# Optimization experiments

Measured on AMD Instinct MI355X. Metric: run time of the kernel, lower is better.

## Reference

```python
import jax, jax.numpy as jnp
import numpy as np

B, T, D, H = 512, 128, 128, 2048  # batch, seq_len, input/output dim, hidden dim
W_SCALE = 0.02


def setup_inputs() -> dict:
    key = jax.random.key(0)
    ks = jax.random.split(key, 4)
    return {
        "tgt": jax.random.normal(ks[0], (B, T, D), jnp.float32),
        "W_ih": jax.random.normal(ks[1], (4 * H, D), jnp.float32) * W_SCALE,
        "W_hh": jax.random.normal(ks[2], (4 * H, H), jnp.float32) * W_SCALE,
        "b_ih": jnp.zeros((4 * H,), jnp.float32),
        "b_hh": jnp.zeros((4 * H,), jnp.float32),
        "W_out": jax.random.normal(ks[3], (D, H), jnp.float32) * W_SCALE,
        "b_out": jnp.zeros((D,), jnp.float32),
    }


def reference(tgt, W_ih, W_hh, b_ih, b_hh, W_out, b_out):
    # LSTMDecoder.forward with teacher_forcing_ratio=0.0 (deterministic,
    # tgt: [B, T, D]; first frame tgt[:, 0] seeds the decoder.
    batch, max_len, _ = tgt.shape
    hidden = W_hh.shape[1]
    b = b_ih + b_hh  # fuse the two LSTM biases

    def step(carry, _):
        x, h, c = carry
        # torch nn.LSTM gate order: i, f, g, o
        gates = x @ W_ih.T + h @ W_hh.T + b  # [B, 4H]
        i, f, g, o = jnp.split(gates, 4, axis=-1)
        c = jax.nn.sigmoid(f) * c + jax.nn.sigmoid(i) * jnp.tanh(g)
        h = jax.nn.sigmoid(o) * jnp.tanh(c)
        out = h @ W_out.T + b_out  # [B, D]
        return (out, h, c), out

    h0 = jnp.zeros((batch, hidden), tgt.dtype)
    c0 = jnp.zeros((batch, hidden), tgt.dtype)
    _, outs = jax.lax.scan(step, (tgt[:, 0, :], h0, c0), None, length=max_len)
    return outs.transpose(1, 0, 2)  # [B, T, D]
```

## Files before the change

kernel.cpp:

```cpp
#include <hip/hip_runtime.h>
#include <hip/hip_fp16.h>

typedef _Float16 f16;
typedef __attribute__((ext_vector_type(8))) _Float16 f16x8;
typedef __attribute__((ext_vector_type(16))) float f32x16;

#define GLL(src, dst) __builtin_amdgcn_global_load_lds( \
    (const __attribute__((address_space(1))) void*)(src), \
    (__attribute__((address_space(3))) void*)(dst), 16, 0, 0)

__device__ __forceinline__ size_t foff(int r, int k, int nkb) {
    return ((size_t)((r >> 5) * nkb + (k >> 4)) << 9)
         + (size_t)(((((k >> 3) & 1)) << 8) + ((r & 31) << 3) + (k & 7));
}

__device__ __forceinline__ void rgemm(
    const f16* __restrict__ pA,
    const f16* __restrict__ pB0, const f16* __restrict__ pB1,
    f16* sB, int wv, int lane, int n, f32x16 acc[2])
{
    #pragma unroll
    for (int nt = 0; nt < 2; ++nt)
      #pragma unroll
      for (int e = 0; e < 16; ++e)
        acc[nt][e] = 0.f;

    const f16* pBs = (wv >> 1) ? pB1 : pB0;
    const int jb = (wv & 1) * 2;
    f16* dst0 = sB + (wv >> 1) * 2048 + jb * 512;

    f16x8 X[4], Y[4];
    auto LA = [&](f16x8 (&R)[4], int t) {
        size_t o = (size_t)t * 2048;
        R[0] = *(const f16x8*)(pA + o);
        R[1] = *(const f16x8*)(pA + o + 512);
        R[2] = *(const f16x8*)(pA + o + 1024);
        R[3] = *(const f16x8*)(pA + o + 1536);
    };
    auto BG = [&](int buf, int t) {
        size_t o = (size_t)t * 2048 + (size_t)jb * 512;
        GLL(pBs + o,       dst0 + buf * 4096);
        GLL(pBs + o + 512, dst0 + buf * 4096 + 512);
    };
    auto STEP = [&](f16x8 (&R)[4], int buf, int t, bool last) {
        if (last) asm volatile("s_waitcnt vmcnt(0)" ::: "memory");
        else      asm volatile("s_waitcnt vmcnt(6)" ::: "memory");
        __builtin_amdgcn_sched_barrier(0);
        __builtin_amdgcn_s_barrier();
        __builtin_amdgcn_sched_barrier(0);
        f16x8 bf[2][4];
        const f16* bb = sB + buf * 4096 + lane * 8;
        #pragma unroll
        for (int nt = 0; nt < 2; ++nt)
          #pragma unroll
          for (int kk = 0; kk < 4; ++kk)
            bf[nt][kk] = *(const f16x8*)(bb + nt * 2048 + kk * 512);
        asm volatile("s_waitcnt lgkmcnt(0)" ::: "memory");
        __builtin_amdgcn_sched_barrier(0);
        __builtin_amdgcn_s_barrier();
        __builtin_amdgcn_sched_barrier(0);
        if (t + 2 < n) BG(buf, t + 2);
        __builtin_amdgcn_s_setprio(1);
        #pragma unroll
        for (int kk = 0; kk < 4; ++kk)
          #pragma unroll
          for (int nt = 0; nt < 2; ++nt)
            acc[nt] = __builtin_amdgcn_mfma_f32_32x32x16_f16(
                R[kk], bf[nt][kk], acc[nt], 0, 0, 0);
        __builtin_amdgcn_s_setprio(0);
        if (t + 2 < n) LA(R, t + 2);
    };

    __builtin_amdgcn_sched_barrier(0);
    BG(0, 0); LA(X, 0);
    __builtin_amdgcn_sched_barrier(0);
    BG(1, 1); LA(Y, 1);
    __builtin_amdgcn_sched_barrier(0);
    for (int t = 0; t < n; t += 2) {
        STEP(X, 0, t, false);
        STEP(Y, 1, t + 1, t + 2 >= n);
    }
}

#define PICKV(ii) ((ii) == 0 ? w0[e] : (ii) == 1 ? w1[e] : (ii) == 2 ? w2[e] : w3[e])

__global__ __launch_bounds__(256, 2) void k_step(
    const f16* __restrict__ Af, int nkb,
    const f16* __restrict__ Bf,
    const float* __restrict__ bias,
    float* __restrict__ Cst,
    f16* __restrict__ Hout)
{
    __shared__ alignas(16) f16 sB[8192];
    const int P = blockIdx.x;
    const int L = (P & 7) * ((int)gridDim.x >> 3) + (P >> 3);
    const int cg = L >> 2, rg = L & 3;
    const int tid = threadIdx.x;
    const int wv = tid >> 6, lane = tid & 63;
    const int l31 = lane & 31, hi = lane >> 5;
    const int mb = rg * 4 + wv;
    const f16* pA  = Af + ((size_t)mb * nkb) * 512 + lane * 8;
    const f16* pB0 = Bf + ((size_t)(cg * 2) * nkb) * 512 + lane * 8;
    const f16* pB1 = pB0 + (size_t)nkb * 512;
    f32x16 acc[2];
    rgemm(pA, pB0, pB1, sB, wv, lane, nkb >> 2, acc);

    const int g = l31 & 3;
    #pragma unroll
    for (int nt = 0; nt < 2; ++nt) {
        const int hid = cg * 16 + nt * 8 + (l31 >> 2);
        const float bown = bias[(g << 11) + hid];
        float w0[16], w1[16], w2[16], w3[16];
        #pragma unroll
        for (int e = 0; e < 16; ++e) {
            float x = acc[nt][e] + bown;
            float xx = (g == 2) ? 2.f * x : x;
            float s = 1.f / (1.f + __expf(-xx));
            w0[e] = (g == 2) ? 2.f * s - 1.f : s;
        }
        #pragma unroll
        for (int e = 0; e < 16; ++e) {
            w1[e] = __shfl_xor(w0[e], 1);
            w2[e] = __shfl_xor(w0[e], 2);
            w3[e] = __shfl_xor(w0[e], 3);
        }
        const int rowb = rg * 128 + wv * 32 + 4 * hi;
        #pragma unroll
        for (int eg = 0; eg < 4; ++eg) {
            if (g == eg) {
                #pragma unroll
                for (int q = 0; q < 4; ++q) {
                    const int e = eg * 4 + q;
                    const float iv = PICKV(eg ^ 0);
                    const float fv = PICKV(eg ^ 1);
                    const float gv = PICKV(eg ^ 2);
                    const float ov = PICKV(eg ^ 3);
                    const int row = rowb + q + 8 * eg;
                    const size_t cidx = (size_t)row * 2048 + hid;
                    const float c = fv * Cst[cidx] + iv * gv;
                    Cst[cidx] = c;
                    Hout[foff(row, hid, 128)] = (f16)(ov * tanhf(c));
                }
            }
        }
    }
}

__global__ __launch_bounds__(256, 2) void k_out(
    const f16* __restrict__ Hbase, const f16* __restrict__ Bf,
    const float* __restrict__ bout, float* __restrict__ out,
    int t0, int rgshift)
{
    __shared__ alignas(16) f16 sB[8192];
    const int P = blockIdx.x;
    const int L = (P & 7) * ((int)gridDim.x >> 3) + (P >> 3);
    const int cg = L >> rgshift;
    const int rg = L & ((1 << rgshift) - 1);
    const int tid = threadIdx.x;
    const int wv = tid >> 6, lane = tid & 63;
    const int l31 = lane & 31, hi = lane >> 5;
    const int m0 = rg * 128 + wv * 32;
    const int slot = m0 >> 9, mloc32 = (m0 & 511) >> 5;
    const f16* pA  = Hbase + (size_t)slot * 1048576
                   + ((size_t)mloc32 * 128) * 512 + lane * 8;
    const f16* pB0 = Bf + ((size_t)(cg * 2) * 128) * 512 + lane * 8;
    const f16* pB1 = pB0 + (size_t)128 * 512;
    f32x16 acc[2];
    rgemm(pA, pB0, pB1, sB, wv, lane, 32, acc);

    #pragma unroll
    for (int nt = 0; nt < 2; ++nt) {
        const int d = cg * 64 + nt * 32 + l31;
        const float bo = bout[d];
        #pragma unroll
        for (int e = 0; e < 16; ++e) {
            const int m = m0 + (e & 3) + 8 * (e >> 2) + 4 * hi;
            out[(size_t)(m & 511) * 16384 + (size_t)(t0 + (m >> 9)) * 128 + d]
                = acc[nt][e] + bo;
        }
    }
}

__global__ __launch_bounds__(256, 2) void k_wcomb(
    const f16* __restrict__ Af,
    const f16* __restrict__ Bf,
    const float* __restrict__ Whh, f16* __restrict__ Wf)
{
    __shared__ alignas(16) f16 sB[8192];
    const int P = blockIdx.x;
    const int L = (P & 7) * ((int)gridDim.x >> 3) + (P >> 3);
    const int cg = L >> 6, rg = L & 63;
    const int tid = threadIdx.x;
    const int wv = tid >> 6, lane = tid & 63;
    const int l31 = lane & 31, hi = lane >> 5;
    const int mb = rg * 4 + wv;
    const f16* pA  = Af + ((size_t)mb * 8) * 512 + lane * 8;
    const f16* pB0 = Bf + ((size_t)(cg * 2) * 8) * 512 + lane * 8;
    const f16* pB1 = pB0 + (size_t)8 * 512;
    f32x16 acc[2];
    rgemm(pA, pB0, pB1, sB, wv, lane, 2, acc);

    #pragma unroll
    for (int nt = 0; nt < 2; ++nt) {
        const int kc = cg * 64 + nt * 32 + l31;
        #pragma unroll
        for (int e = 0; e < 16; ++e) {
            const int r = rg * 128 + wv * 32 + (e & 3) + 8 * (e >> 2) + 4 * hi;
            const float v = acc[nt][e] + Whh[(size_t)r * 2048 + kc];
            const int rho = ((r & 2047) << 2) | (r >> 11);
            Wf[foff(rho, kc, 128)] = (f16)v;
        }
    }
}


__global__ void k_x0f(const float* __restrict__ tgt, f16* __restrict__ x0f)
{
    int i = blockIdx.x * 256 + threadIdx.x;
    int b = i >> 7, k = i & 127;
    x0f[foff(b, k, 8)] = (f16)tgt[(size_t)b * 16384 + k];
}

__global__ void k_wihf(const float* __restrict__ Wih, f16* __restrict__ Wihf)
{
    int i = blockIdx.x * 256 + threadIdx.x;
    int rho = i >> 7, k = i & 127;
    int gate = rho & 3, hid = rho >> 2;
    Wihf[foff(rho, k, 8)] = (f16)Wih[((size_t)gate * 2048 + hid) * 128 + k];
}

__global__ void k_wihaf(const float* __restrict__ Wih, f16* __restrict__ Wihaf)
{
    int i = blockIdx.x * 256 + threadIdx.x;
    int r = i >> 7, k = i & 127;
    Wihaf[foff(r, k, 8)] = (f16)Wih[(size_t)r * 128 + k];
}

__global__ void k_woutTf(const float* __restrict__ Wout, f16* __restrict__ WoutTf)
{
    int i = blockIdx.x * 256 + threadIdx.x;
    int d = i >> 11, n = i & 2047;
    WoutTf[foff(n, d, 8)] = (f16)Wout[(size_t)d * 2048 + n];
}

__global__ void k_woutf(const float* __restrict__ Wout, f16* __restrict__ Woutf)
{
    int i = blockIdx.x * 256 + threadIdx.x;
    int d = i >> 11, k = i & 2047;
    Woutf[foff(d, k, 128)] = (f16)Wout[(size_t)d * 2048 + k];
}

__global__ void k_bias(const float* __restrict__ bih, const float* __restrict__ bhh,
                       const float* __restrict__ Wih, const float* __restrict__ bout,
                       float* __restrict__ b0, float* __restrict__ bp)
{
    int r = blockIdx.x * 256 + threadIdx.x;
    if (r >= 8192) return;
    float s = bih[r] + bhh[r];
    float a = 0.f;
    for (int d = 0; d < 128; ++d) a += Wih[(size_t)r * 128 + d] * bout[d];
    b0[r] = s;
    bp[r] = s + a;
}


extern "C" void kernel_launch(void* const* d_in, const int* in_sizes, int n_in,
                              void* d_out, int out_size, void* d_ws, size_t ws_size,
                              hipStream_t stream)
{
    const float* tgt  = (const float*)d_in[0];
    const float* Wih  = (const float*)d_in[1];
    const float* Whh  = (const float*)d_in[2];
    const float* bih  = (const float*)d_in[3];
    const float* bhh  = (const float*)d_in[4];
    const float* Wout = (const float*)d_in[5];
    const float* bout = (const float*)d_in[6];
    float* out = (float*)d_out;

    char* ws = (char*)d_ws;
    size_t off = 0;
    auto alloc = [&](size_t bytes) -> void* {
        void* p = ws + off;
        off += (bytes + 255) & ~(size_t)255;
        return p;
    };
    f16*   Wf     = (f16*)alloc((size_t)8192 * 2048 * 2);
    f16*   Wihf   = (f16*)alloc((size_t)8192 * 128 * 2);
    f16*   Wihaf  = (f16*)alloc((size_t)8192 * 128 * 2);
    f16*   WoutTf = (f16*)alloc((size_t)2048 * 128 * 2);
    f16*   Woutf  = (f16*)alloc((size_t)128 * 2048 * 2);
    f16*   x0f    = (f16*)alloc((size_t)512 * 128 * 2);
    float* b0     = (float*)alloc(8192 * 4);
    float* bp     = (float*)alloc(8192 * 4);
    float* Cst    = (float*)alloc((size_t)512 * 2048 * 4);

    const size_t slotsz = (size_t)512 * 2048;
    int depth = 0;
    const int cands[7] = {128, 64, 32, 16, 8, 4, 2};
    for (int i = 0; i < 7; ++i)
        if (off + (size_t)cands[i] * slotsz * 2 <= ws_size) { depth = cands[i]; break; }
    if (depth == 0) return;
    f16* Hbuf = (f16*)alloc((size_t)depth * slotsz * 2);
    const int rgshift = __builtin_ctz((unsigned)(depth * 4));

    hipMemsetAsync(Cst, 0, (size_t)512 * 2048 * 4, stream);
    k_x0f   <<<dim3(256),  dim3(256), 0, stream>>>(tgt, x0f);
    k_wihf  <<<dim3(4096), dim3(256), 0, stream>>>(Wih, Wihf);
    k_wihaf <<<dim3(4096), dim3(256), 0, stream>>>(Wih, Wihaf);
    k_woutTf<<<dim3(1024), dim3(256), 0, stream>>>(Wout, WoutTf);
    k_woutf <<<dim3(1024), dim3(256), 0, stream>>>(Wout, Woutf);
    k_bias  <<<dim3(32),   dim3(256), 0, stream>>>(bih, bhh, Wih, bout, b0, bp);
    k_wcomb <<<dim3(2048), dim3(256), 0, stream>>>(Wihaf, WoutTf, Whh, Wf);

    k_step<<<dim3(512), dim3(256), 0, stream>>>(x0f, 8, Wihf, b0, Cst, Hbuf);
    for (int s = 1; s < 128; ++s) {
        if ((s % depth) == 0)
            k_out<<<dim3(8 * depth), dim3(256), 0, stream>>>(
                Hbuf, Woutf, bout, out, s - depth, rgshift);
        k_step<<<dim3(512), dim3(256), 0, stream>>>(
            Hbuf + (size_t)((s - 1) % depth) * slotsz, 128, Wf, bp,
            Cst, Hbuf + (size_t)(s % depth) * slotsz);
    }
    k_out<<<dim3(8 * depth), dim3(256), 0, stream>>>(
        Hbuf, Woutf, bout, out, 128 - depth, rgshift);
}
```

Baseline: 4.538 ms.

## Deepen GEMM software pipeline to four LDS buffers with a single barrier

The inner recurrent GEMM moves from a 2-stage to a 4-stage pipeline. It uses four register sets for A fragments and four LDS buffers for B tiles, prefetching 3–4 k-steps ahead. The second workgroup barrier per step is removed, since the buffer being refilled is no longer the one being read. LDS per block doubles to 32 KB and register pressure rises, which could lower occupancy or cause spills. Any benefit depends on how much latency was still exposed in the memory-bound recurrent step.

Result: faster. 4.408 ms (-2.9%).

```diff
diff --git a/kernel.cpp b/kernel.cpp
--- a/kernel.cpp
+++ b/kernel.cpp
@@ -8,6 +8,7 @@
 #define GLL(src, dst) __builtin_amdgcn_global_load_lds( \
     (const __attribute__((address_space(1))) void*)(src), \
     (__attribute__((address_space(3))) void*)(dst), 16, 0, 0)
+#define SB0() __builtin_amdgcn_sched_barrier(0)
 
 __device__ __forceinline__ size_t foff(int r, int k, int nkb) {
     return ((size_t)((r >> 5) * nkb + (k >> 4)) << 9)
@@ -29,7 +30,7 @@
     const int jb = (wv & 1) * 2;
     f16* dst0 = sB + (wv >> 1) * 2048 + jb * 512;
 
-    f16x8 X[4], Y[4];
+    f16x8 R0[4], R1[4], R2[4], R3[4];
     auto LA = [&](f16x8 (&R)[4], int t) {
         size_t o = (size_t)t * 2048;
         R[0] = *(const f16x8*)(pA + o);
@@ -42,12 +43,17 @@
         GLL(pBs + o,       dst0 + buf * 4096);
         GLL(pBs + o + 512, dst0 + buf * 4096 + 512);
     };
-    auto STEP = [&](f16x8 (&R)[4], int buf, int t, bool last) {
-        if (last) asm volatile("s_waitcnt vmcnt(0)" ::: "memory");
-        else      asm volatile("s_waitcnt vmcnt(6)" ::: "memory");
-        __builtin_amdgcn_sched_barrier(0);
+    auto STEP = [&](f16x8 (&R)[4], int buf, int t) {
+        const int r = n - 1 - t;
+        if (r >= 3)      asm volatile("s_waitcnt vmcnt(16)" ::: "memory");
+        else if (r == 2) asm volatile("s_waitcnt vmcnt(12)" ::: "memory");
+        else if (r == 1) asm volatile("s_waitcnt vmcnt(6)"  ::: "memory");
+        else             asm volatile("s_waitcnt vmcnt(0)"  ::: "memory");
+        SB0();
         __builtin_amdgcn_s_barrier();
-        __builtin_amdgcn_sched_barrier(0);
+        SB0();
+        if (t + 3 < n) BG((t + 3) & 3, t + 3);
+        SB0();
         f16x8 bf[2][4];
         const f16* bb = sB + buf * 4096 + lane * 8;
         #pragma unroll
@@ -56,10 +62,7 @@
           for (int kk = 0; kk < 4; ++kk)
             bf[nt][kk] = *(const f16x8*)(bb + nt * 2048 + kk * 512);
         asm volatile("s_waitcnt lgkmcnt(0)" ::: "memory");
-        __builtin_amdgcn_sched_barrier(0);
-        __builtin_amdgcn_s_barrier();
-        __builtin_amdgcn_sched_barrier(0);
-        if (t + 2 < n) BG(buf, t + 2);
+        SB0();
         __builtin_amdgcn_s_setprio(1);
         #pragma unroll
         for (int kk = 0; kk < 4; ++kk)
@@ -68,17 +71,25 @@
             acc[nt] = __builtin_amdgcn_mfma_f32_32x32x16_f16(
                 R[kk], bf[nt][kk], acc[nt], 0, 0, 0);
         __builtin_amdgcn_s_setprio(0);
-        if (t + 2 < n) LA(R, t + 2);
+        SB0();
+        if (t + 4 < n) LA(R, t + 4);
+        SB0();
     };
 
-    __builtin_amdgcn_sched_barrier(0);
-    BG(0, 0); LA(X, 0);
-    __builtin_amdgcn_sched_barrier(0);
-    BG(1, 1); LA(Y, 1);
-    __builtin_amdgcn_sched_barrier(0);
-    for (int t = 0; t < n; t += 2) {
-        STEP(X, 0, t, false);
-        STEP(Y, 1, t + 1, t + 2 >= n);
+    SB0();
+    BG(0, 0); LA(R0, 0);
+    SB0();
+    if (1 < n) { BG(1, 1); LA(R1, 1); }
+    SB0();
+    if (2 < n) { BG(2, 2); LA(R2, 2); }
+    SB0();
+    if (3 < n) LA(R3, 3);
+    SB0();
+    for (int t = 0; t < n; t += 4) {
+        STEP(R0, 0, t);
+        if (t + 1 < n) STEP(R1, 1, t + 1);
+        if (t + 2 < n) STEP(R2, 2, t + 2);
+        if (t + 3 < n) STEP(R3, 3, t + 3);
     }
 }
 
@@ -91,7 +102,7 @@
     float* __restrict__ Cst,
     f16* __restrict__ Hout)
 {
-    __shared__ alignas(16) f16 sB[8192];
+    __shared__ alignas(16) f16 sB[16384];
     const int P = blockIdx.x;
     const int L = (P & 7) * ((int)gridDim.x >> 3) + (P >> 3);
     const int cg = L >> 2, rg = L & 3;
@@ -151,7 +162,7 @@
     const float* __restrict__ bout, float* __restrict__ out,
     int t0, int rgshift)
 {
-    __shared__ alignas(16) f16 sB[8192];
+    __shared__ alignas(16) f16 sB[16384];
     const int P = blockIdx.x;
     const int L = (P & 7) * ((int)gridDim.x >> 3) + (P >> 3);
     const int cg = L >> rgshift;
@@ -186,7 +197,7 @@
     const f16* __restrict__ Bf,
     const float* __restrict__ Whh, f16* __restrict__ Wf)
 {
-    __shared__ alignas(16) f16 sB[8192];
+    __shared__ alignas(16) f16 sB[16384];
     const int P = blockIdx.x;
     const int L = (P & 7) * ((int)gridDim.x >> 3) + (P >> 3);
     const int cg = L >> 6, rg = L & 63;
```
